# Kernel tuning notes

Measured on AMD Instinct MI355X. Metric: run time of the kernel, lower is better.

Reference implementation:

```python
import jax, jax.numpy as jnp
import numpy as np

B, IN, OUT = 4096, 512, 512
NUM_KNOTS, DEGREE = 10, 3


def setup_inputs() -> dict:
    key = jax.random.key(0)
    k1, k2 = jax.random.split(key)
    x = jax.random.normal(k1, (B, IN), dtype=jnp.float32)
    # coefficients of all out*in edge splines: [out, in, num_knots-1, degree+1]
    coeff = jax.random.normal(k2, (OUT, IN, NUM_KNOTS - 1, DEGREE + 1), dtype=jnp.float32) * 0.1
    scale = jnp.ones((OUT,), dtype=jnp.float32)
    return {"x": x, "coeff": coeff, "scale": scale}


def reference(x, coeff, scale):
    # x: [B, IN]; coeff: [OUT, IN, S, P]; scale: [OUT]
    out_f, in_f, S, P = coeff.shape
    K = S + 1
    knots = jnp.linspace(-1.0, 1.0, K)            # shared uniform knots
    xc = jnp.clip(x, -1.0, 1.0)
    seg = jnp.clip(jnp.searchsorted(knots[1:], xc), 0, S - 1)  # [B, IN]
    lo = knots[seg]
    t = (xc - lo) / (knots[seg + 1] - lo)          # [B, IN]
    tpow = t[..., None] ** jnp.arange(P, dtype=x.dtype)        # [B, IN, P]
    onehot = jax.nn.one_hot(seg, S, dtype=x.dtype)             # [B, IN, S]
    # A[b,i,s,p] = onehot * t^p ; contraction with coeff is a single GEMM
    A = onehot[..., :, None] * tpow[..., None, :]              # [B, IN, S, P]
    y = jnp.einsum('bisp,jisp->bj', A, coeff)                  # [B, OUT]
    return y * scale
```

## Files before the change

### kernel.cpp

```cpp
#include <hip/hip_runtime.h>

#define B_DIM   4096
#define IN_DIM  512
#define OUT_DIM 512
#define KTOT    (IN_DIM * 36)
#define BM      128
#define BN      128
#define BK      64
#define KSPLIT  8
#define KPER    (KTOT / KSPLIT)
#define STEPS   (KPER / BK)

using f32x4 = __attribute__((ext_vector_type(4))) float;
using s16x8 = __attribute__((ext_vector_type(8))) short;
using u32x4 = __attribute__((ext_vector_type(4))) unsigned int;

__device__ __forceinline__ unsigned int f2bf(float f) {
    unsigned int u = __float_as_uint(f);
    return (u + 0x7FFFu + ((u >> 16) & 1u)) >> 16;
}

__device__ __forceinline__ void glds16(const void* g, void* l) {
    __builtin_amdgcn_global_load_lds(
        (const __attribute__((address_space(1))) unsigned int*)g,
        (__attribute__((address_space(3))) unsigned int*)l,
        16, 0, 0);
}

__device__ __forceinline__ uint2 spline_rec_packed(float xv) {
    float xc = fminf(fmaxf(xv, -1.0f), 1.0f);
    double xd = (double)xc;
    int s = 0;
#pragma unroll
    for (int k = 1; k <= 8; ++k)
        s += ((-1.0 + (double)k * (2.0 / 9.0)) < xd) ? 1 : 0;
    double lo = -1.0 + (double)s * (2.0 / 9.0);
    double hi = -1.0 + (double)(s + 1) * (2.0 / 9.0);
    float t  = (float)((xd - lo) / (hi - lo));
    float t2 = t * t, t3 = t2 * t;
    uint2 r;
    r.x = f2bf(t)  | (f2bf(t2) << 16);
    r.y = f2bf(t3) | ((unsigned int)s << 16);
    return r;
}

__global__ void prep_x_kernel(const float* __restrict__ x, uint2* __restrict__ tp) {
    int idx = blockIdx.x * 256 + threadIdx.x;
    if (idx >= B_DIM * IN_DIM) return;
    tp[idx] = spline_rec_packed(x[idx]);
}

__global__ void prep_coeff_kernel(const float* __restrict__ c,
                                  const float* __restrict__ scale,
                                  u32x4* __restrict__ cbf) {
    int idx = blockIdx.x * 256 + threadIdx.x;
    if (idx >= (OUT_DIM * KTOT) / 8) return;
    long base = (long)idx * 8;
    int  j = (int)(base / KTOT);
    float s = scale[j];
    f32x4 a = *(const f32x4*)(c + base);
    f32x4 b = *(const f32x4*)(c + base + 4);
    u32x4 o;
    o.x = f2bf(a.x * s) | (f2bf(a.y * s) << 16);
    o.y = f2bf(a.z * s) | (f2bf(a.w * s) << 16);
    o.z = f2bf(b.x * s) | (f2bf(b.y * s) << 16);
    o.w = f2bf(b.z * s) | (f2bf(b.w * s) << 16);
    cbf[idx] = o;
}

__device__ __forceinline__ void scat(char* AsB, int ar, int ah, uint2 rec, int i, int k0) {
    if (i * 36 < k0 + BK && i < IN_DIM) {
        int s   = (int)(rec.y >> 16);
        int off = i * 36 + s * 4 - k0;
        if (off >= 0 && off <= 60) {
            int oct = off >> 3;
            if ((oct >> 2) == ah) {
                uint2 w;
                w.x = 0x3F80u | (rec.x << 16);
                w.y = (rec.x >> 16) | (rec.y << 16);
                *(uint2*)(AsB + oct * 2048 + ar * 16 + ((off >> 2) & 1) * 8) = w;
            }
        }
    }
}

__device__ __forceinline__ void load_recs(const uint2* __restrict__ tpRow, int k0,
                                          uint2& q0, uint2& q1, uint2& q2) {
    int ifirst = k0 / 36;
    q0 = tpRow[ifirst];
    q1 = tpRow[ifirst + 1];
    q2 = tpRow[ifirst + 2 < IN_DIM ? ifirst + 2 : 0];
}

__launch_bounds__(256, 4)
__global__ void kan_gemm_fast(const unsigned short* __restrict__ cbf,
                              const uint2* __restrict__ tp,
                              float* __restrict__ out) {
    __shared__ unsigned short AsF[8 * BM * 8];
    __shared__ unsigned short BsF[8 * BN * 8];

    const int tid  = threadIdx.x;
    const int lane = tid & 63;
    const int wave = tid >> 6;
    const int wm = wave >> 1, wn = wave & 1;
    const int l15 = lane & 15, lhi = lane >> 4;

    const int bid = blockIdx.x;
    const int nt = bid & 3;
    const int ks = (bid >> 2) & 7;
    const int mt = bid >> 5;
    const int m0g = mt * BM, n0g = nt * BN, kbase = ks * KPER;

    const int ar = tid >> 1;
    const int ah = tid & 1;
    const int bjg = n0g + (tid & 127);
    const int tidHi = tid >> 7;

    char* AsB = (char*)AsF;
    char* BsB = (char*)BsF;
    const uint2* tpRow = tp + (long)(m0g + ar) * IN_DIM;
    const char*  bRow  = (const char*)cbf + (long)bjg * (KTOT * 2);

    uint2 r0, r1, r2;
    load_recs(tpRow, kbase, r0, r1, r2);

    f32x4 acc[4][4] = {};

    for (int step = 0; step < STEPS; ++step) {
        const int k0 = kbase + step * BK;

        u32x4 z = {};
#pragma unroll
        for (int zi = 0; zi < 4; ++zi)
            *(u32x4*)(AsB + (ah * 4 + zi) * 2048 + ar * 16) = z;
        {
            const int ifirst = k0 / 36;
            scat(AsB, ar, ah, r0, ifirst,     k0);
            scat(AsB, ar, ah, r1, ifirst + 1, k0);
            scat(AsB, ar, ah, r2, ifirst + 2, k0);
        }

#pragma unroll
        for (int it = 0; it < 4; ++it) {
            const int q    = it * 256 + tid;
            const int koct = it * 2 + tidHi;
            glds16(bRow + (long)(k0 + koct * 8) * 2, BsB + q * 16);
        }

        __syncthreads();

        if (step + 1 < STEPS)
            load_recs(tpRow, k0 + BK, r0, r1, r2);

#pragma unroll
        for (int kh = 0; kh < 2; ++kh) {
            s16x8 a[4], b[4];
#pragma unroll
            for (int mf = 0; mf < 4; ++mf)
                a[mf] = *(const s16x8*)(AsB + (kh * 4 + lhi) * 2048 + (wm * 64 + mf * 16 + l15) * 16);
#pragma unroll
            for (int nf = 0; nf < 4; ++nf)
                b[nf] = *(const s16x8*)(BsB + (kh * 4 + lhi) * 2048 + (wn * 64 + nf * 16 + l15) * 16);
#pragma unroll
            for (int mf = 0; mf < 4; ++mf)
#pragma unroll
                for (int nf = 0; nf < 4; ++nf)
                    acc[mf][nf] = __builtin_amdgcn_mfma_f32_16x16x32_bf16(a[mf], b[nf], acc[mf][nf], 0, 0, 0);
        }

        __syncthreads();
    }

#pragma unroll
    for (int mf = 0; mf < 4; ++mf) {
        const int cmBase = m0g + wm * 64 + mf * 16 + lhi * 4;
#pragma unroll
        for (int nf = 0; nf < 4; ++nf) {
            const int cn = n0g + wn * 64 + nf * 16 + l15;
#pragma unroll
            for (int e = 0; e < 4; ++e)
                atomicAdd(out + (long)(cmBase + e) * OUT_DIM + cn, acc[mf][nf][e]);
        }
    }
}

#define FKPER  4608
#define FSTEPS 72
__launch_bounds__(256, 2)
__global__ void kan_gemm_ref(const float* __restrict__ x,
                             const float* __restrict__ coeff,
                             const float* __restrict__ scale,
                             float* __restrict__ out) {
    __shared__ unsigned short AsF[BM * 72];
    __shared__ unsigned short BsF[8 * BN * 8];
    const int tid  = threadIdx.x;
    const int lane = tid & 63;
    const int wave = tid >> 6;
    const int wm = wave >> 1, wn = wave & 1;
    const int l15 = lane & 15, lhi = lane >> 4;
    const int bid = blockIdx.x;
    const int nt = bid & 3;
    const int ks = (bid >> 2) & 3;
    const int mt = bid >> 4;
    const int m0g = mt * BM, n0g = nt * BN, kbase = ks * FKPER;
    const int ar = tid >> 1, ah = tid & 1;
    const int abrow = m0g + ar;
    const int bjg = n0g + (tid & 127);
    const float bscale = scale[bjg];
    char* AsB = (char*)AsF;
    char* BsB = (char*)BsF;
    f32x4 acc[4][4] = {};
    for (int step = 0; step < FSTEPS; ++step) {
        const int k0 = kbase + step * BK;
        {
            char* rb = AsB + ar * 144;
            u32x4 z = {};
            if (ah == 0) {
#pragma unroll
                for (int z4 = 0; z4 < 4; ++z4) *(u32x4*)(rb + z4 * 16) = z;
            } else {
#pragma unroll
                for (int z4 = 4; z4 < 9; ++z4) *(u32x4*)(rb + z4 * 16) = z;
            }
            const int ifirst = k0 / 36;
#pragma unroll
            for (int ii = 0; ii < 2; ++ii) {
                const int cand = ah + ii * 2;
                const int i = ifirst + cand;
                if (cand < 3 && i * 36 < k0 + BK && i < IN_DIM) {
                    uint2 rec = spline_rec_packed(x[(long)abrow * IN_DIM + i]);
                    int s = (int)(rec.y >> 16);
                    const int off = i * 36 + s * 4 - k0;
                    unsigned int w0 = 0x3F80u | (rec.x << 16);
                    unsigned int w1 = (rec.x >> 16) | (rec.y << 16);
                    if (off >= 0 && off <= 62) *(unsigned int*)(rb + off * 2) = w0;
                    const int off2 = off + 2;
                    if (off2 >= 0 && off2 <= 62) *(unsigned int*)(rb + off2 * 2) = w1;
                }
            }
        }
#pragma unroll
        for (int it = 0; it < 4; ++it) {
            const int q  = it * 256 + tid;
            const int c  = q >> 7;
            const int kk = k0 + c * 8;
            f32x4 a = *(const f32x4*)(coeff + (long)bjg * KTOT + kk);
            f32x4 b = *(const f32x4*)(coeff + (long)bjg * KTOT + kk + 4);
            u32x4 o;
            o.x = f2bf(a.x * bscale) | (f2bf(a.y * bscale) << 16);
            o.y = f2bf(a.z * bscale) | (f2bf(a.w * bscale) << 16);
            o.z = f2bf(b.x * bscale) | (f2bf(b.y * bscale) << 16);
            o.w = f2bf(b.z * bscale) | (f2bf(b.w * bscale) << 16);
            *(u32x4*)(BsB + q * 16) = o;
        }
        __syncthreads();
#pragma unroll
        for (int kh = 0; kh < 2; ++kh) {
            const int kk = kh * 32;
            s16x8 a[4], b[4];
#pragma unroll
            for (int mf = 0; mf < 4; ++mf)
                a[mf] = *(const s16x8*)(AsB + (wm * 64 + mf * 16 + l15) * 144 + (kk + lhi * 8) * 2);
#pragma unroll
            for (int nf = 0; nf < 4; ++nf)
                b[nf] = *(const s16x8*)(BsB + (kh * 4 + lhi) * 2048 + (wn * 64 + nf * 16 + l15) * 16);
#pragma unroll
            for (int mf = 0; mf < 4; ++mf)
#pragma unroll
                for (int nf = 0; nf < 4; ++nf)
                    acc[mf][nf] = __builtin_amdgcn_mfma_f32_16x16x32_bf16(a[mf], b[nf], acc[mf][nf], 0, 0, 0);
        }
        __syncthreads();
    }
#pragma unroll
    for (int mf = 0; mf < 4; ++mf) {
        const int cmBase = m0g + wm * 64 + mf * 16 + lhi * 4;
#pragma unroll
        for (int nf = 0; nf < 4; ++nf) {
            const int cn = n0g + wn * 64 + nf * 16 + l15;
#pragma unroll
            for (int e = 0; e < 4; ++e)
                atomicAdd(out + (long)(cmBase + e) * OUT_DIM + cn, acc[mf][nf][e]);
        }
    }
}

extern "C" void kernel_launch(void* const* d_in, const int* in_sizes, int n_in,
                              void* d_out, int out_size, void* d_ws, size_t ws_size,
                              hipStream_t stream) {
    const float* x     = (const float*)d_in[0];
    const float* coeff = (const float*)d_in[1];
    const float* scale = (const float*)d_in[2];
    float* out = (float*)d_out;

    const size_t SZ_CBF = (size_t)OUT_DIM * KTOT * 2;
    const size_t SZ_TP  = (size_t)B_DIM * IN_DIM * 8;
    const size_t NEED   = SZ_CBF + SZ_TP;

    hipMemsetAsync(d_out, 0, (size_t)B_DIM * OUT_DIM * sizeof(float), stream);

    if (ws_size >= NEED) {
        unsigned short* cbf = (unsigned short*)d_ws;
        uint2*          tp  = (uint2*)((char*)d_ws + SZ_CBF);
        prep_coeff_kernel<<<4608, 256, 0, stream>>>(coeff, scale, (u32x4*)cbf);
        prep_x_kernel<<<8192, 256, 0, stream>>>(x, tp);
        kan_gemm_fast<<<1024, 256, 0, stream>>>(cbf, tp, out);
    } else {
        kan_gemm_ref<<<512, 256, 0, stream>>>(x, coeff, scale, out);
    }
}
```

Baseline: 157.5 us.

## Double-buffer LDS tiles and pre-tile bf16 coefficients for contiguous loads

The GEMM kernel now uses two LDS buffers for the A and B tiles. While MFMAs consume the current tile, the next tile's A scatter and B global-to-LDS loads are issued, and the spline records for the tile after that are prefetched. The coefficient prep kernel writes bf16 coefficients in a tile-major layout, so each 64-wide K tile for 128 output columns is one contiguous 16KB block. This is meant to hide load latency and improve coalescing. In exchange, LDS use doubles to 64KB and occupancy is lowered to 2 blocks per CU.

```diff
diff --git a/kernel.cpp b/kernel.cpp
--- a/kernel.cpp
+++ b/kernel.cpp
@@ -3,13 +3,11 @@
 #define B_DIM   4096
 #define IN_DIM  512
 #define OUT_DIM 512
-#define KTOT    (IN_DIM * 36)
-#define BM      128
-#define BN      128
+#define KTOT    18432
 #define BK      64
 #define KSPLIT  8
-#define KPER    (KTOT / KSPLIT)
-#define STEPS   (KPER / BK)
+#define KPER    2304
+#define NT      36
 
 using f32x4 = __attribute__((ext_vector_type(4))) float;
 using s16x8 = __attribute__((ext_vector_type(8))) short;
@@ -50,54 +48,56 @@
     tp[idx] = spline_rec_packed(x[idx]);
 }
 
-__global__ void prep_coeff_kernel(const float* __restrict__ c,
-                                  const float* __restrict__ scale,
-                                  u32x4* __restrict__ cbf) {
-    int idx = blockIdx.x * 256 + threadIdx.x;
-    if (idx >= (OUT_DIM * KTOT) / 8) return;
-    long base = (long)idx * 8;
-    int  j = (int)(base / KTOT);
+__global__ void prep_coeff2(const float* __restrict__ c,
+                            const float* __restrict__ scale,
+                            u32x4* __restrict__ cbf2) {
+    int g = blockIdx.x * 256 + threadIdx.x;
+    if (g >= (OUT_DIM * KTOT) / 8) return;
+    int row = g & 127;
+    int oct = (g >> 7) & 7;
+    int hi  = g >> 10;
+    int ntg = hi / 288;
+    int kt  = hi - ntg * 288;
+    int j = ntg * 128 + row;
+    int k = kt * 64 + oct * 8;
     float s = scale[j];
-    f32x4 a = *(const f32x4*)(c + base);
-    f32x4 b = *(const f32x4*)(c + base + 4);
+    const float* src = c + (size_t)j * KTOT + k;
+    f32x4 a = *(const f32x4*)src;
+    f32x4 b = *(const f32x4*)(src + 4);
     u32x4 o;
     o.x = f2bf(a.x * s) | (f2bf(a.y * s) << 16);
     o.y = f2bf(a.z * s) | (f2bf(a.w * s) << 16);
     o.z = f2bf(b.x * s) | (f2bf(b.y * s) << 16);
     o.w = f2bf(b.z * s) | (f2bf(b.w * s) << 16);
-    cbf[idx] = o;
-}
-
-__device__ __forceinline__ void scat(char* AsB, int ar, int ah, uint2 rec, int i, int k0) {
-    if (i * 36 < k0 + BK && i < IN_DIM) {
-        int s   = (int)(rec.y >> 16);
-        int off = i * 36 + s * 4 - k0;
-        if (off >= 0 && off <= 60) {
-            int oct = off >> 3;
-            if ((oct >> 2) == ah) {
+    cbf2[g] = o;
+}
+
+__device__ __forceinline__ void scat3(char* Aq, int ar, int ah,
+                                      uint2 q0, uint2 q1, uint2 q2,
+                                      int ifirst, int k0) {
+#pragma unroll
+    for (int cc = 0; cc < 3; ++cc) {
+        uint2 rec = cc == 0 ? q0 : (cc == 1 ? q1 : q2);
+        int i = ifirst + cc;
+        if (i < IN_DIM) {
+            int s = (int)(rec.y >> 16);
+            int off = i * 36 + s * 4 - k0;
+            if (off >= 0 && off < 64 && ((off >> 5) == ah)) {
                 uint2 w;
                 w.x = 0x3F80u | (rec.x << 16);
                 w.y = (rec.x >> 16) | (rec.y << 16);
-                *(uint2*)(AsB + oct * 2048 + ar * 16 + ((off >> 2) & 1) * 8) = w;
+                *(uint2*)(Aq + (off >> 3) * 2048 + ar * 16 + (off & 4) * 2) = w;
             }
         }
     }
 }
 
-__device__ __forceinline__ void load_recs(const uint2* __restrict__ tpRow, int k0,
-                                          uint2& q0, uint2& q1, uint2& q2) {
-    int ifirst = k0 / 36;
-    q0 = tpRow[ifirst];
-    q1 = tpRow[ifirst + 1];
-    q2 = tpRow[ifirst + 2 < IN_DIM ? ifirst + 2 : 0];
-}
-
-__launch_bounds__(256, 4)
-__global__ void kan_gemm_fast(const unsigned short* __restrict__ cbf,
-                              const uint2* __restrict__ tp,
-                              float* __restrict__ out) {
-    __shared__ unsigned short AsF[8 * BM * 8];
-    __shared__ unsigned short BsF[8 * BN * 8];
+__launch_bounds__(256, 2)
+__global__ void kan_gemm_db(const unsigned short* __restrict__ cbf2,
+                            const uint2* __restrict__ tp,
+                            float* __restrict__ out) {
+    __shared__ u32x4 ldsRaw[65536 / 16];
+    char* lds = (char*)ldsRaw;
 
     const int tid  = threadIdx.x;
     const int lane = tid & 63;
@@ -109,58 +109,73 @@
     const int nt = bid & 3;
     const int ks = (bid >> 2) & 7;
     const int mt = bid >> 5;
-    const int m0g = mt * BM, n0g = nt * BN, kbase = ks * KPER;
-
-    const int ar = tid >> 1;
-    const int ah = tid & 1;
-    const int bjg = n0g + (tid & 127);
-    const int tidHi = tid >> 7;
-
-    char* AsB = (char*)AsF;
-    char* BsB = (char*)BsF;
-    const uint2* tpRow = tp + (long)(m0g + ar) * IN_DIM;
-    const char*  bRow  = (const char*)cbf + (long)bjg * (KTOT * 2);
-
+    const int m0g = mt * 128, n0g = nt * 128;
+    const int kbase = ks * KPER;
+
+    const int ar = tid & 127, ah = tid >> 7;
+
+    const uint2* tpRow = tp + (size_t)(m0g + ar) * IN_DIM;
+    const char*  cbase = (const char*)cbf2 + (size_t)(nt * 288 + ks * NT) * 16384;
+
+    f32x4 acc[4][4] = {};
     uint2 r0, r1, r2;
-    load_recs(tpRow, kbase, r0, r1, r2);
-
-    f32x4 acc[4][4] = {};
-
-    for (int step = 0; step < STEPS; ++step) {
-        const int k0 = kbase + step * BK;
-
+
+    {
+        char* A0 = lds;
+        char* B0 = lds + 32768;
+        const int if0 = kbase / 36;
+        uint2 q0 = tpRow[if0];
+        uint2 q1 = tpRow[if0 + 1 < IN_DIM ? if0 + 1 : IN_DIM - 1];
+        uint2 q2 = tpRow[if0 + 2 < IN_DIM ? if0 + 2 : IN_DIM - 1];
         u32x4 z = {};
 #pragma unroll
         for (int zi = 0; zi < 4; ++zi)
-            *(u32x4*)(AsB + (ah * 4 + zi) * 2048 + ar * 16) = z;
-        {
-            const int ifirst = k0 / 36;
-            scat(AsB, ar, ah, r0, ifirst,     k0);
-            scat(AsB, ar, ah, r1, ifirst + 1, k0);
-            scat(AsB, ar, ah, r2, ifirst + 2, k0);
-        }
-
-#pragma unroll
-        for (int it = 0; it < 4; ++it) {
-            const int q    = it * 256 + tid;
-            const int koct = it * 2 + tidHi;
-            glds16(bRow + (long)(k0 + koct * 8) * 2, BsB + q * 16);
-        }
-
+            *(u32x4*)(A0 + (ah * 4 + zi) * 2048 + ar * 16) = z;
+        scat3(A0, ar, ah, q0, q1, q2, if0, kbase);
+#pragma unroll
+        for (int it = 0; it < 4; ++it)
+            glds16(cbase + it * 4096 + tid * 16, B0 + it * 4096 + tid * 16);
+        const int if1 = (kbase + BK) / 36;
+        r0 = tpRow[if1];
+        r1 = tpRow[if1 + 1 < IN_DIM ? if1 + 1 : IN_DIM - 1];
+        r2 = tpRow[if1 + 2 < IN_DIM ? if1 + 2 : IN_DIM - 1];
         __syncthreads();
-
-        if (step + 1 < STEPS)
-            load_recs(tpRow, k0 + BK, r0, r1, r2);
+    }
+
+    for (int t = 0; t < NT; ++t) {
+        const int p = t & 1;
+        const char* Ap = lds + p * 16384;
+        const char* Bp = lds + 32768 + p * 16384;
+        char* Aq = lds + (p ^ 1) * 16384;
+        char* Bq = lds + 32768 + (p ^ 1) * 16384;
+
+        if (t + 1 < NT) {
+            const int k0n = kbase + (t + 1) * BK;
+            u32x4 z = {};
+#pragma unroll
+            for (int zi = 0; zi < 4; ++zi)
+                *(u32x4*)(Aq + (ah * 4 + zi) * 2048 + ar * 16) = z;
+            scat3(Aq, ar, ah, r0, r1, r2, k0n / 36, k0n);
+            const char* srcT = cbase + (size_t)(t + 1) * 16384;
+#pragma unroll
+            for (int it = 0; it < 4; ++it)
+                glds16(srcT + it * 4096 + tid * 16, Bq + it * 4096 + tid * 16);
+            const int tn = t + 2 < NT ? t + 2 : NT - 1;
+            const int ifn = (kbase + tn * BK) / 36;
+            r0 = tpRow[ifn];
+            r1 = tpRow[ifn + 1 < IN_DIM ? ifn + 1 : IN_DIM - 1];
+            r2 = tpRow[ifn + 2 < IN_DIM ? ifn + 2 : IN_DIM - 1];
+        }
 
 #pragma unroll
         for (int kh = 0; kh < 2; ++kh) {
             s16x8 a[4], b[4];
 #pragma unroll
             for (int mf = 0; mf < 4; ++mf)
-                a[mf] = *(const s16x8*)(AsB + (kh * 4 + lhi) * 2048 + (wm * 64 + mf * 16 + l15) * 16);
+                a[mf] = *(const s16x8*)(Ap + (kh * 4 + lhi) * 2048 + (wm * 64 + mf * 16 + l15) * 16);
 #pragma unroll
             for (int nf = 0; nf < 4; ++nf)
-                b[nf] = *(const s16x8*)(BsB + (kh * 4 + lhi) * 2048 + (wn * 64 + nf * 16 + l15) * 16);
+                b[nf] = *(const s16x8*)(Bp + (kh * 4 + lhi) * 2048 + (wn * 64 + nf * 16 + l15) * 16);
 #pragma unroll
             for (int mf = 0; mf < 4; ++mf)
 #pragma unroll
@@ -173,17 +188,19 @@
 
 #pragma unroll
     for (int mf = 0; mf < 4; ++mf) {
-        const int cmBase = m0g + wm * 64 + mf * 16 + lhi * 4;
+        const int rg = m0g + wm * 64 + mf * 16 + lhi * 4;
 #pragma unroll
         for (int nf = 0; nf < 4; ++nf) {
-            const int cn = n0g + wn * 64 + nf * 16 + l15;
+            const int cg = n0g + wn * 64 + nf * 16 + l15;
 #pragma unroll
             for (int e = 0; e < 4; ++e)
-                atomicAdd(out + (long)(cmBase + e) * OUT_DIM + cn, acc[mf][nf][e]);
-        }
-    }
-}
-
+                atomicAdd(out + (size_t)(rg + e) * OUT_DIM + cg, acc[mf][nf][e]);
+        }
+    }
+}
+
+#define BM 128
+#define BN 128
 #define FKPER  4608
 #define FSTEPS 72
 __launch_bounds__(256, 2)
@@ -228,7 +245,7 @@
                 const int cand = ah + ii * 2;
                 const int i = ifirst + cand;
                 if (cand < 3 && i * 36 < k0 + BK && i < IN_DIM) {
-                    uint2 rec = spline_rec_packed(x[(long)abrow * IN_DIM + i]);
+                    uint2 rec = spline_rec_packed(x[(size_t)abrow * IN_DIM + i]);
                     int s = (int)(rec.y >> 16);
                     const int off = i * 36 + s * 4 - k0;
                     unsigned int w0 = 0x3F80u | (rec.x << 16);
@@ -244,8 +261,8 @@
             const int q  = it * 256 + tid;
             const int c  = q >> 7;
             const int kk = k0 + c * 8;
-            f32x4 a = *(const f32x4*)(coeff + (long)bjg * KTOT + kk);
-            f32x4 b = *(const f32x4*)(coeff + (long)bjg * KTOT + kk + 4);
+            f32x4 a = *(const f32x4*)(coeff + (size_t)bjg * KTOT + kk);
+            f32x4 b = *(const f32x4*)(coeff + (size_t)bjg * KTOT + kk + 4);
             u32x4 o;
             o.x = f2bf(a.x * bscale) | (f2bf(a.y * bscale) << 16);
             o.y = f2bf(a.z * bscale) | (f2bf(a.w * bscale) << 16);
@@ -280,7 +297,7 @@
             const int cn = n0g + wn * 64 + nf * 16 + l15;
 #pragma unroll
             for (int e = 0; e < 4; ++e)
-                atomicAdd(out + (long)(cmBase + e) * OUT_DIM + cn, acc[mf][nf][e]);
+                atomicAdd(out + (size_t)(cmBase + e) * OUT_DIM + cn, acc[mf][nf][e]);
         }
     }
 }
@@ -300,11 +317,11 @@
     hipMemsetAsync(d_out, 0, (size_t)B_DIM * OUT_DIM * sizeof(float), stream);
 
     if (ws_size >= NEED) {
-        unsigned short* cbf = (unsigned short*)d_ws;
-        uint2*          tp  = (uint2*)((char*)d_ws + SZ_CBF);
-        prep_coeff_kernel<<<4608, 256, 0, stream>>>(coeff, scale, (u32x4*)cbf);
+        unsigned short* cbf2 = (unsigned short*)d_ws;
+        uint2*          tp   = (uint2*)((char*)d_ws + SZ_CBF);
+        prep_coeff2<<<4608, 256, 0, stream>>>(coeff, scale, (u32x4*)cbf2);
         prep_x_kernel<<<8192, 256, 0, stream>>>(x, tp);
-        kan_gemm_fast<<<1024, 256, 0, stream>>>(cbf, tp, out);
+        kan_gemm_db<<<1024, 256, 0, stream>>>(cbf2, tp, out);
     } else {
         kan_gemm_ref<<<512, 256, 0, stream>>>(x, coeff, scale, out);
     }
```

Result: slower. 176.0 us (+11.7%).
